# Optimization experiments

Hardware: AMD Instinct MI355X
Metric: run time of the kernel (lower is better)

Reference implementation:

```python
import jax, jax.numpy as jnp
import numpy as np

B = 32768
T = 1024  # num_time_bins


def setup_inputs() -> dict:
    key = jax.random.key(0)
    k1, k2, k3, k4 = jax.random.split(key, 4)
    hazard_values = jax.random.uniform(k1, (B, T), dtype=jnp.float32)
    labels_Y = jax.random.uniform(k2, (B,), dtype=jnp.float32) * T
    # nn.Linear(T, T): weight [T, T] (out, in), bias [T]
    lim = 1.0 / np.sqrt(T)
    W = jax.random.uniform(k3, (T, T), minval=-lim, maxval=lim, dtype=jnp.float32)
    b = jax.random.uniform(k4, (T,), minval=-lim, maxval=lim, dtype=jnp.float32)
    return {"hazard_values": hazard_values, "labels_Y": labels_Y, "W": W, "b": b}


def reference(hazard_values, labels_Y, W, b):
    # linear + sigmoid + argmax -> per-row truncation position
    logits = hazard_values @ W.T + b                       # [B, T]
    trunc_pos = jnp.argmax(jax.nn.sigmoid(logits), axis=1, keepdims=True)  # [B, 1] int
    # survival curve
    S = jnp.cumprod(1.0 - hazard_values, axis=1)           # [B, T]
    # vectorized truncation decay: for t >= p, multiply by exp(-(t - p))
    t = jnp.arange(T)[None, :]                             # [1, T]
    decay = jnp.where(t >= trunc_pos,
                      jnp.exp(-(t - trunc_pos).astype(S.dtype)),
                      jnp.ones((), S.dtype))
    S = S * decay
    # MSE between argmax position and labels (original prints; we skip prints)
    p = trunc_pos[:, 0].astype(jnp.float32)
    truncation_loss = jnp.mean((p - labels_Y) ** 2)
    return trunc_pos, S, truncation_loss
```

## Files before the change

### kernel.cpp

```cpp
#include <hip/hip_runtime.h>

#define B_ROWS 32768
#define T_BINS 1024

typedef __attribute__((ext_vector_type(8))) _Float16 half8;
typedef __attribute__((ext_vector_type(4))) float floatx4;

__device__ __forceinline__ unsigned long long pack_max(float v, int col) {
    unsigned x = __float_as_uint(v);
    x = (x & 0x80000000u) ? ~x : (x | 0x80000000u);
    return ((unsigned long long)x << 32) | (unsigned)(~col);
}

__device__ __forceinline__ void async16h(const _Float16* g, _Float16* l) {
    __builtin_amdgcn_global_load_lds(
        (const __attribute__((address_space(1))) unsigned int*)g,
        (__attribute__((address_space(3))) unsigned int*)l,
        16, 0, 0);
}

__global__ __launch_bounds__(256) void tof16_kernel(
    const float* __restrict__ src, _Float16* __restrict__ dst, int n4)
{
    int idx = blockIdx.x * 256 + threadIdx.x;
    if (idx >= n4) return;
    float4 x = ((const float4*)src)[idx];
    union { _Float16 h[4]; ushort4 u; } cv;
    cv.h[0] = (_Float16)x.x;
    cv.h[1] = (_Float16)x.y;
    cv.h[2] = (_Float16)x.z;
    cv.h[3] = (_Float16)x.w;
    ((ushort4*)dst)[idx] = cv.u;
}

__global__ __launch_bounds__(256, 2) void mega_kernel(
    const float* __restrict__ A, const _Float16* __restrict__ Wh,
    const float* __restrict__ bias, const float* __restrict__ labels,
    float* __restrict__ out_trunc, float* __restrict__ out_S,
    float* __restrict__ loss_acc)
{
    __shared__ _Float16 sA[2][64 * 64];
    __shared__ _Float16 sW[2][256 * 64];

    const int tid  = threadIdx.x;
    const int lane = tid & 63;
    const int wc   = tid >> 6;
    const int by   = blockIdx.x;

    const int arow = tid >> 2;
    const int ac   = tid & 3;
    const int x8a  = (arow ^ (arow >> 3)) & 7;
    const int sAw0 = arow * 64 + (((ac * 2) ^ x8a) * 8);
    const int sAw1 = arow * 64 + (((ac * 2 + 1) ^ x8a) * 8);
    const float* Abase = A + (size_t)(by * 64 + arow) * T_BINS + ac * 16;

    const int l3   = lane >> 3;
    const int wsl  = lane & 7;

    const int l15  = lane & 15;
    const int hi   = lane >> 4;
    const int xc   = (l15 & 7) ^ (l15 >> 3);

    float run_best[4][4];
    int   run_col[4][4];
#pragma unroll
    for (int i = 0; i < 4; ++i)
#pragma unroll
        for (int r = 0; r < 4; ++r) { run_best[i][r] = -3.4e38f; run_col[i][r] = 0; }

    {
        float4 f0 = *(const float4*)(Abase + 0);
        float4 f1 = *(const float4*)(Abase + 4);
        float4 f2 = *(const float4*)(Abase + 8);
        float4 f3 = *(const float4*)(Abase + 12);
        half8 h0, h1;
        h0[0] = (_Float16)f0.x; h0[1] = (_Float16)f0.y; h0[2] = (_Float16)f0.z; h0[3] = (_Float16)f0.w;
        h0[4] = (_Float16)f1.x; h0[5] = (_Float16)f1.y; h0[6] = (_Float16)f1.z; h0[7] = (_Float16)f1.w;
        h1[0] = (_Float16)f2.x; h1[1] = (_Float16)f2.y; h1[2] = (_Float16)f2.z; h1[3] = (_Float16)f2.w;
        h1[4] = (_Float16)f3.x; h1[5] = (_Float16)f3.y; h1[6] = (_Float16)f3.z; h1[7] = (_Float16)f3.w;
        *(half8*)&sA[0][sAw0] = h0;
        *(half8*)&sA[0][sAw1] = h1;
    }
#pragma unroll
    for (int r = 0; r < 8; ++r)
        async16h(Wh + (size_t)(wc * 64 + r * 8 + l3) * T_BINS + ((wsl ^ l3 ^ r) * 8),
                 &sW[0][(wc * 64 + r * 8) * 64]);
    float4 pa0 = *(const float4*)(Abase + 64);
    float4 pa1 = *(const float4*)(Abase + 68);
    float4 pa2 = *(const float4*)(Abase + 72);
    float4 pa3 = *(const float4*)(Abase + 76);
    __syncthreads();

    int n = 0;
    for (int bx = 0; bx < 4; ++bx) {
        const int colbase = bx * 256 + wc * 64 + l15;
        float bj[4];
#pragma unroll
        for (int j = 0; j < 4; ++j) bj[j] = bias[colbase + j * 16];

        floatx4 acc[4][4];
#pragma unroll
        for (int i = 0; i < 4; ++i)
#pragma unroll
            for (int j = 0; j < 4; ++j) acc[i][j] = (floatx4){0.f, 0.f, 0.f, 0.f};

        for (int t = 0; t < 16; ++t, ++n) {
            const int cur = n & 1;
            const int nxt = cur ^ 1;
            const int m   = (n + 1) & 63;
            const int bxn = m >> 4;
            const int k0n = (m & 15) * 64;

            const int kq = ((n + 2) & 15) * 64;
            float4 qa0 = *(const float4*)(Abase + kq + 0);
            float4 qa1 = *(const float4*)(Abase + kq + 4);
            float4 qa2 = *(const float4*)(Abase + kq + 8);
            float4 qa3 = *(const float4*)(Abase + kq + 12);

#pragma unroll
            for (int r = 0; r < 8; ++r)
                async16h(Wh + (size_t)(bxn * 256 + wc * 64 + r * 8 + l3) * T_BINS
                            + k0n + ((wsl ^ l3 ^ r) * 8),
                         &sW[nxt][(wc * 64 + r * 8) * 64]);

            {
                half8 h0, h1;
                h0[0] = (_Float16)pa0.x; h0[1] = (_Float16)pa0.y; h0[2] = (_Float16)pa0.z; h0[3] = (_Float16)pa0.w;
                h0[4] = (_Float16)pa1.x; h0[5] = (_Float16)pa1.y; h0[6] = (_Float16)pa1.z; h0[7] = (_Float16)pa1.w;
                h1[0] = (_Float16)pa2.x; h1[1] = (_Float16)pa2.y; h1[2] = (_Float16)pa2.z; h1[3] = (_Float16)pa2.w;
                h1[4] = (_Float16)pa3.x; h1[5] = (_Float16)pa3.y; h1[6] = (_Float16)pa3.z; h1[7] = (_Float16)pa3.w;
                *(half8*)&sA[nxt][sAw0] = h0;
                *(half8*)&sA[nxt][sAw1] = h1;
            }
            pa0 = qa0; pa1 = qa1; pa2 = qa2; pa3 = qa3;

#pragma unroll
            for (int g = 0; g < 2; ++g) {
                half8 ah[4], whf[4];
#pragma unroll
                for (int i = 0; i < 4; ++i)
                    ah[i] = *(const half8*)&sA[cur][(i * 16 + l15) * 64
                                                    + (((g * 4 + hi) ^ xc ^ (i * 2)) * 8)];
#pragma unroll
                for (int j = 0; j < 4; ++j)
                    whf[j] = *(const half8*)&sW[cur][(wc * 64 + j * 16 + l15) * 64
                                                     + (((g * 4 + hi) ^ xc ^ (j * 2)) * 8)];
#pragma unroll
                for (int i = 0; i < 4; ++i)
#pragma unroll
                    for (int j = 0; j < 4; ++j)
                        acc[i][j] = __builtin_amdgcn_mfma_f32_16x16x32_f16(ah[i], whf[j], acc[i][j], 0, 0, 0);
            }

            __syncthreads();
        }

#pragma unroll
        for (int i = 0; i < 4; ++i)
#pragma unroll
            for (int r = 0; r < 4; ++r)
#pragma unroll
                for (int j = 0; j < 4; ++j) {
                    float v = acc[i][j][r] + bj[j];
                    if (v > run_best[i][r]) { run_best[i][r] = v; run_col[i][r] = colbase + j * 16; }
                }
    }

    unsigned long long (*cand)[64] = reinterpret_cast<unsigned long long (*)[64]>(&sA[0][0]);
    float* trunc_s = reinterpret_cast<float*>(&sA[0][0]) + 512;

#pragma unroll
    for (int i = 0; i < 4; ++i)
#pragma unroll
        for (int r = 0; r < 4; ++r) {
            float best = run_best[i][r];
            int   bc   = run_col[i][r];
#pragma unroll
            for (int off = 8; off >= 1; off >>= 1) {
                float ov = __shfl_xor(best, off, 64);
                int   oc = __shfl_xor(bc, off, 64);
                if (ov > best || (ov == best && oc < bc)) { best = ov; bc = oc; }
            }
            if ((lane & 15) == 0)
                cand[wc][i * 16 + (lane >> 4) * 4 + r] = pack_max(best, bc);
        }
    __syncthreads();

    if (tid < 64) {
        unsigned long long m01 = cand[0][tid] > cand[1][tid] ? cand[0][tid] : cand[1][tid];
        unsigned long long m23 = cand[2][tid] > cand[3][tid] ? cand[2][tid] : cand[3][tid];
        unsigned long long mm = m01 > m23 ? m01 : m23;
        unsigned col = ~(unsigned)mm;
        float p = (float)col;
        int rowG = by * 64 + tid;
        out_trunc[rowG] = p;
        trunc_s[tid] = p;
        float d = p - labels[rowG];
        float term = d * d * (1.0f / (float)B_ROWS);
#pragma unroll
        for (int off = 32; off >= 1; off >>= 1)
            term += __shfl_down(term, off, 64);
        if (tid == 0) atomicAdd(loss_acc, term);
    }
    __syncthreads();

    for (int rr = 0; rr < 16; ++rr) {
        int row  = wc * 16 + rr;
        int rowG = by * 64 + row;
        const float* Hrow = A + (size_t)rowG * T_BINS + lane * 16;
        float4 h0 = *(const float4*)(Hrow + 0);
        float4 h1 = *(const float4*)(Hrow + 4);
        float4 h2 = *(const float4*)(Hrow + 8);
        float4 h3 = *(const float4*)(Hrow + 12);
        float hv[16] = {h0.x, h0.y, h0.z, h0.w, h1.x, h1.y, h1.z, h1.w,
                        h2.x, h2.y, h2.z, h2.w, h3.x, h3.y, h3.z, h3.w};
        float vprod[16];
        float run = 1.f;
#pragma unroll
        for (int j = 0; j < 16; ++j) { run *= (1.f - hv[j]); vprod[j] = run; }
        float x = run;
#pragma unroll
        for (int off = 1; off < 64; off <<= 1) {
            float o = __shfl_up(x, off, 64);
            if (lane >= off) x *= o;
        }
        float pre = __shfl_up(x, 1, 64);
        if (lane == 0) pre = 1.f;

        int p  = (int)trunc_s[row];
        int t0 = lane * 16;
        float sv[16];
#pragma unroll
        for (int j = 0; j < 16; ++j) {
            float s = pre * vprod[j];
            int t = t0 + j;
            if (t >= p) s *= __expf((float)(p - t));
            sv[j] = s;
        }
        float* Srow = out_S + (size_t)rowG * T_BINS + lane * 16;
        *(float4*)(Srow + 0)  = (float4){sv[0],  sv[1],  sv[2],  sv[3]};
        *(float4*)(Srow + 4)  = (float4){sv[4],  sv[5],  sv[6],  sv[7]};
        *(float4*)(Srow + 8)  = (float4){sv[8],  sv[9],  sv[10], sv[11]};
        *(float4*)(Srow + 12) = (float4){sv[12], sv[13], sv[14], sv[15]};
    }
}

#define BMf 64
#define BKf 16
#define LDSS (BMf + 4)
__global__ __launch_bounds__(256) void gemm_argmax_fp32(
    const float* __restrict__ A, const float* __restrict__ W,
    const float* __restrict__ bias, unsigned long long* __restrict__ rec)
{
    __shared__ float As[BKf][LDSS];
    __shared__ float Ws[BKf][LDSS];
    const int tid = threadIdx.x;
    const int tx = tid & 15, ty = tid >> 4;
    const int bx = blockIdx.x, by = blockIdx.y;
    const int ar = tid >> 2, ak = (tid & 3) << 2;
    const float* Arow = A + (size_t)(by * BMf + ar) * T_BINS + ak;
    const float* Wrow = W + (size_t)(bx * BMf + ar) * T_BINS + ak;
    float acc[4][4];
#pragma unroll
    for (int i = 0; i < 4; ++i)
#pragma unroll
        for (int j = 0; j < 4; ++j) acc[i][j] = 0.f;
    for (int k0 = 0; k0 < T_BINS; k0 += BKf) {
        float4 av = *(const float4*)(Arow + k0);
        float4 wvv = *(const float4*)(Wrow + k0);
        As[ak + 0][ar] = av.x; As[ak + 1][ar] = av.y; As[ak + 2][ar] = av.z; As[ak + 3][ar] = av.w;
        Ws[ak + 0][ar] = wvv.x; Ws[ak + 1][ar] = wvv.y; Ws[ak + 2][ar] = wvv.z; Ws[ak + 3][ar] = wvv.w;
        __syncthreads();
#pragma unroll
        for (int k = 0; k < BKf; ++k) {
            float4 a4 = *(const float4*)&As[k][ty * 4];
            float4 w4 = *(const float4*)&Ws[k][tx * 4];
            float aa[4] = {a4.x, a4.y, a4.z, a4.w};
            float ww[4] = {w4.x, w4.y, w4.z, w4.w};
#pragma unroll
            for (int i = 0; i < 4; ++i)
#pragma unroll
                for (int j = 0; j < 4; ++j) acc[i][j] = fmaf(aa[i], ww[j], acc[i][j]);
        }
        __syncthreads();
    }
    const int colBase = bx * BMf + tx * 4;
    float bv[4];
#pragma unroll
    for (int j = 0; j < 4; ++j) bv[j] = bias[colBase + j];
#pragma unroll
    for (int i = 0; i < 4; ++i) {
        float best = acc[i][0] + bv[0];
        int bc = colBase;
#pragma unroll
        for (int j = 1; j < 4; ++j) {
            float v = acc[i][j] + bv[j];
            if (v > best) { best = v; bc = colBase + j; }
        }
#pragma unroll
        for (int off = 8; off >= 1; off >>= 1) {
            float ov = __shfl_xor(best, off, 64);
            int oc = __shfl_xor(bc, off, 64);
            if (ov > best || (ov == best && oc < bc)) { best = ov; bc = oc; }
        }
        if (tx == 0) atomicMax(&rec[by * BMf + ty * 4 + i], pack_max(best, bc));
    }
}

__global__ __launch_bounds__(256) void finalize_kernel(
    const unsigned long long* __restrict__ rec, const float* __restrict__ labels,
    float* __restrict__ out_trunc, float* __restrict__ loss_acc)
{
    int i = blockIdx.x * 256 + threadIdx.x;
    unsigned col = ~(unsigned)(rec[i] & 0xFFFFFFFFull);
    float p = (float)col;
    out_trunc[i] = p;
    float d = p - labels[i];
    float term = d * d * (1.0f / (float)B_ROWS);
#pragma unroll
    for (int off = 32; off >= 1; off >>= 1)
        term += __shfl_down(term, off, 64);
    __shared__ float partials[4];
    int lane = threadIdx.x & 63, wv = threadIdx.x >> 6;
    if (lane == 0) partials[wv] = term;
    __syncthreads();
    if (threadIdx.x == 0)
        atomicAdd(loss_acc, partials[0] + partials[1] + partials[2] + partials[3]);
}

__global__ __launch_bounds__(256) void scan_kernel_f32(
    const float* __restrict__ H, const float* __restrict__ trunc_f,
    float* __restrict__ Sout)
{
    const int row = blockIdx.x;
    const int tid = threadIdx.x;
    const int lane = tid & 63;
    const int wv = tid >> 6;
    const float4 h = *(const float4*)(H + (size_t)row * T_BINS + tid * 4);
    float l0 = 1.f - h.x;
    float l1 = l0 * (1.f - h.y);
    float l2 = l1 * (1.f - h.z);
    float l3 = l2 * (1.f - h.w);
    float x = l3;
#pragma unroll
    for (int off = 1; off < 64; off <<= 1) {
        float o = __shfl_up(x, off, 64);
        if (lane >= off) x *= o;
    }
    float ex = __shfl_up(x, 1, 64);
    if (lane == 0) ex = 1.f;
    __shared__ float wtot[4];
    if (lane == 63) wtot[wv] = x;
    __syncthreads();
    float wpre = 1.f;
#pragma unroll
    for (int w = 0; w < 3; ++w)
        if (w < wv) wpre *= wtot[w];
    float pre = wpre * ex;
    int p = (int)trunc_f[row];
    int t0 = tid * 4;
    float sv[4] = {pre * l0, pre * l1, pre * l2, pre * l3};
#pragma unroll
    for (int j = 0; j < 4; ++j) {
        int t = t0 + j;
        if (t >= p) sv[j] *= __expf((float)(p - t));
    }
    float4 s4 = {sv[0], sv[1], sv[2], sv[3]};
    *(float4*)(Sout + (size_t)row * T_BINS + tid * 4) = s4;
}

extern "C" void kernel_launch(void* const* d_in, const int* in_sizes, int n_in,
                              void* d_out, int out_size, void* d_ws, size_t ws_size,
                              hipStream_t stream)
{
    const float* hazard = (const float*)d_in[0];
    const float* labels = (const float*)d_in[1];
    const float* W      = (const float*)d_in[2];
    const float* bias   = (const float*)d_in[3];

    float* out       = (float*)d_out;
    float* out_trunc = out;
    float* out_S     = out + B_ROWS;
    float* out_loss  = out + B_ROWS + (size_t)B_ROWS * T_BINS;

    hipMemsetAsync(out_loss, 0, sizeof(float), stream);

    const size_t NW = (size_t)T_BINS * T_BINS;
    if (ws_size >= NW * sizeof(_Float16)) {
        _Float16* Wh = (_Float16*)d_ws;
        tof16_kernel<<<(int)(NW / 4 / 256), 256, 0, stream>>>(W, Wh, (int)(NW / 4));
        mega_kernel<<<B_ROWS / 64, 256, 0, stream>>>(
            hazard, Wh, bias, labels, out_trunc, out_S, out_loss);
    } else {
        unsigned long long* rec = (unsigned long long*)out_S;
        hipMemsetAsync(rec, 0, (size_t)B_ROWS * sizeof(unsigned long long), stream);
        dim3 ggrid(T_BINS / BMf, B_ROWS / BMf);
        gemm_argmax_fp32<<<ggrid, 256, 0, stream>>>(hazard, W, bias, rec);
        finalize_kernel<<<B_ROWS / 256, 256, 0, stream>>>(rec, labels, out_trunc, out_loss);
        scan_kernel_f32<<<B_ROWS, 256, 0, stream>>>(hazard, out_trunc, out_S);
    }
}
```

Before: 352.8 us.

## Split fused kernel into large-tile fp16 GEMM-argmax and separate scan kernel

Replaces the single mega kernel with a 256x256-tile fp16 MFMA GEMM that reduces the per-row argmax across column quarters through 64-bit atomicMax records in workspace. A second kernel decodes the records, computes the loss and writes the truncated survival curves. The larger tiles raise operand reuse in the GEMM, and 512 blocks of 512 threads give better CU occupancy. In exchange, hazard is read twice from HBM and the mega kernel's overlap of the scan with the GEMM is lost.

```diff
diff --git a/kernel.cpp b/kernel.cpp
--- a/kernel.cpp
+++ b/kernel.cpp
@@ -31,6 +31,221 @@
     cv.h[2] = (_Float16)x.z;
     cv.h[3] = (_Float16)x.w;
     ((ushort4*)dst)[idx] = cv.u;
+}
+
+__global__ __launch_bounds__(512, 2) void gemm_argmax_f16(
+    const float* __restrict__ A, const _Float16* __restrict__ Wh,
+    const float* __restrict__ bias, unsigned long long* __restrict__ rec)
+{
+    __shared__ _Float16 sA[2][256 * 64];
+    __shared__ _Float16 sW[2][256 * 64];
+
+    const int tid  = threadIdx.x;
+    const int lane = tid & 63;
+    const int w    = tid >> 6;
+    const int wr   = w >> 1;
+    const int wcl  = w & 1;
+    const int slab = blockIdx.x >> 2;
+    const int cq   = blockIdx.x & 3;
+
+    const int arow = tid >> 1;
+    const int part = tid & 1;
+    const int x8a  = (arow ^ (arow >> 3)) & 7;
+    const float* Abase = A + (size_t)(slab * 256 + arow) * T_BINS;
+
+    const int l3  = lane >> 3;
+    const int wsl = lane & 7;
+
+    const int l15 = lane & 15;
+    const int hi  = lane >> 4;
+
+    floatx4 acc[4][8];
+#pragma unroll
+    for (int i = 0; i < 4; ++i)
+#pragma unroll
+        for (int j = 0; j < 8; ++j) acc[i][j] = (floatx4){0.f, 0.f, 0.f, 0.f};
+
+#pragma unroll
+    for (int s = 0; s < 4; ++s) {
+        int ps = part * 4 + s;
+        int sc = ps ^ x8a;
+        float4 f0 = *(const float4*)(Abase + sc * 8);
+        float4 f1 = *(const float4*)(Abase + sc * 8 + 4);
+        half8 hv;
+        hv[0] = (_Float16)f0.x; hv[1] = (_Float16)f0.y; hv[2] = (_Float16)f0.z; hv[3] = (_Float16)f0.w;
+        hv[4] = (_Float16)f1.x; hv[5] = (_Float16)f1.y; hv[6] = (_Float16)f1.z; hv[7] = (_Float16)f1.w;
+        *(half8*)&sA[0][arow * 64 + ps * 8] = hv;
+    }
+#pragma unroll
+    for (int r = 0; r < 4; ++r) {
+        int cl = w * 32 + r * 8 + l3;
+        int sk = wsl ^ ((cl ^ (cl >> 3)) & 7);
+        async16h(Wh + (size_t)(cq * 256 + cl) * T_BINS + sk * 8,
+                 &sW[0][(w * 32 + r * 8) * 64]);
+    }
+    __syncthreads();
+
+    for (int t = 0; t < 16; ++t) {
+        const int cur = t & 1;
+        const int nxt = cur ^ 1;
+        const int kn  = ((t + 1) & 15) * 64;
+
+        float4 qa0[4], qa1[4];
+#pragma unroll
+        for (int s = 0; s < 4; ++s) {
+            int sc = (part * 4 + s) ^ x8a;
+            qa0[s] = *(const float4*)(Abase + kn + sc * 8);
+            qa1[s] = *(const float4*)(Abase + kn + sc * 8 + 4);
+        }
+
+#pragma unroll
+        for (int r = 0; r < 4; ++r) {
+            int cl = w * 32 + r * 8 + l3;
+            int sk = wsl ^ ((cl ^ (cl >> 3)) & 7);
+            async16h(Wh + (size_t)(cq * 256 + cl) * T_BINS + kn + sk * 8,
+                     &sW[nxt][(w * 32 + r * 8) * 64]);
+        }
+
+#pragma unroll
+        for (int g = 0; g < 2; ++g) {
+            half8 ah[4];
+#pragma unroll
+            for (int i = 0; i < 4; ++i) {
+                int rl = wr * 64 + i * 16 + l15;
+                int xa = (rl ^ (rl >> 3)) & 7;
+                ah[i] = *(const half8*)&sA[cur][rl * 64 + (((g * 4 + hi) ^ xa) * 8)];
+            }
+#pragma unroll
+            for (int jb = 0; jb < 2; ++jb) {
+                half8 whf[4];
+#pragma unroll
+                for (int jj = 0; jj < 4; ++jj) {
+                    int cl = wcl * 128 + (jb * 4 + jj) * 16 + l15;
+                    int xw = (cl ^ (cl >> 3)) & 7;
+                    whf[jj] = *(const half8*)&sW[cur][cl * 64 + (((g * 4 + hi) ^ xw) * 8)];
+                }
+#pragma unroll
+                for (int i = 0; i < 4; ++i)
+#pragma unroll
+                    for (int jj = 0; jj < 4; ++jj)
+                        acc[i][jb * 4 + jj] = __builtin_amdgcn_mfma_f32_16x16x32_f16(
+                            ah[i], whf[jj], acc[i][jb * 4 + jj], 0, 0, 0);
+            }
+        }
+
+#pragma unroll
+        for (int s = 0; s < 4; ++s) {
+            half8 hv;
+            hv[0] = (_Float16)qa0[s].x; hv[1] = (_Float16)qa0[s].y;
+            hv[2] = (_Float16)qa0[s].z; hv[3] = (_Float16)qa0[s].w;
+            hv[4] = (_Float16)qa1[s].x; hv[5] = (_Float16)qa1[s].y;
+            hv[6] = (_Float16)qa1[s].z; hv[7] = (_Float16)qa1[s].w;
+            *(half8*)&sA[nxt][arow * 64 + (part * 4 + s) * 8] = hv;
+        }
+
+        __syncthreads();
+    }
+
+    const int colbase = cq * 256 + wcl * 128 + l15;
+    float bj[8];
+#pragma unroll
+    for (int j = 0; j < 8; ++j) bj[j] = bias[colbase + j * 16];
+
+    unsigned long long (*cand)[256] = reinterpret_cast<unsigned long long (*)[256]>(&sA[0][0]);
+
+#pragma unroll
+    for (int i = 0; i < 4; ++i)
+#pragma unroll
+        for (int r = 0; r < 4; ++r) {
+            float best = -3.4e38f;
+            int   bc   = 0;
+#pragma unroll
+            for (int j = 0; j < 8; ++j) {
+                float v = acc[i][j][r] + bj[j];
+                if (v > best) { best = v; bc = colbase + j * 16; }
+            }
+#pragma unroll
+            for (int off = 8; off >= 1; off >>= 1) {
+                float ov = __shfl_xor(best, off, 64);
+                int   oc = __shfl_xor(bc, off, 64);
+                if (ov > best || (ov == best && oc < bc)) { best = ov; bc = oc; }
+            }
+            if (l15 == 0)
+                cand[wcl][wr * 64 + i * 16 + hi * 4 + r] = pack_max(best, bc);
+        }
+    __syncthreads();
+
+    if (tid < 256) {
+        unsigned long long m0 = cand[0][tid], m1 = cand[1][tid];
+        atomicMax(&rec[slab * 256 + tid], m0 > m1 ? m0 : m1);
+    }
+}
+
+__global__ __launch_bounds__(256) void finscan_kernel(
+    const float* __restrict__ A, const unsigned long long* __restrict__ rec,
+    const float* __restrict__ labels, float* __restrict__ out_trunc,
+    float* __restrict__ out_S, float* __restrict__ loss_acc)
+{
+    __shared__ float trunc_s[64];
+    const int tid  = threadIdx.x;
+    const int lane = tid & 63;
+    const int wc   = tid >> 6;
+    const int by   = blockIdx.x;
+
+    if (tid < 64) {
+        int rowG = by * 64 + tid;
+        unsigned col = ~(unsigned)(rec[rowG] & 0xFFFFFFFFull);
+        float p = (float)col;
+        out_trunc[rowG] = p;
+        trunc_s[tid] = p;
+        float d = p - labels[rowG];
+        float term = d * d * (1.0f / (float)B_ROWS);
+#pragma unroll
+        for (int off = 32; off >= 1; off >>= 1)
+            term += __shfl_down(term, off, 64);
+        if (tid == 0) atomicAdd(loss_acc, term);
+    }
+    __syncthreads();
+
+    for (int rr = 0; rr < 16; ++rr) {
+        int row  = wc * 16 + rr;
+        int rowG = by * 64 + row;
+        const float* Hrow = A + (size_t)rowG * T_BINS + lane * 16;
+        float4 h0 = *(const float4*)(Hrow + 0);
+        float4 h1 = *(const float4*)(Hrow + 4);
+        float4 h2 = *(const float4*)(Hrow + 8);
+        float4 h3 = *(const float4*)(Hrow + 12);
+        float hv[16] = {h0.x, h0.y, h0.z, h0.w, h1.x, h1.y, h1.z, h1.w,
+                        h2.x, h2.y, h2.z, h2.w, h3.x, h3.y, h3.z, h3.w};
+        float vprod[16];
+        float run = 1.f;
+#pragma unroll
+        for (int j = 0; j < 16; ++j) { run *= (1.f - hv[j]); vprod[j] = run; }
+        float x = run;
+#pragma unroll
+        for (int off = 1; off < 64; off <<= 1) {
+            float o = __shfl_up(x, off, 64);
+            if (lane >= off) x *= o;
+        }
+        float pre = __shfl_up(x, 1, 64);
+        if (lane == 0) pre = 1.f;
+
+        int p  = (int)trunc_s[row];
+        int t0 = lane * 16;
+        float sv[16];
+#pragma unroll
+        for (int j = 0; j < 16; ++j) {
+            float s = pre * vprod[j];
+            int t = t0 + j;
+            if (t >= p) s *= __expf((float)(p - t));
+            sv[j] = s;
+        }
+        float* Srow = out_S + (size_t)rowG * T_BINS + lane * 16;
+        *(float4*)(Srow + 0)  = (float4){sv[0],  sv[1],  sv[2],  sv[3]};
+        *(float4*)(Srow + 4)  = (float4){sv[4],  sv[5],  sv[6],  sv[7]};
+        *(float4*)(Srow + 8)  = (float4){sv[8],  sv[9],  sv[10], sv[11]};
+        *(float4*)(Srow + 12) = (float4){sv[12], sv[13], sv[14], sv[15]};
+    }
 }
 
 __global__ __launch_bounds__(256, 2) void mega_kernel(
@@ -386,7 +601,17 @@
     hipMemsetAsync(out_loss, 0, sizeof(float), stream);
 
     const size_t NW = (size_t)T_BINS * T_BINS;
-    if (ws_size >= NW * sizeof(_Float16)) {
+    const size_t wh_bytes  = NW * sizeof(_Float16);
+    const size_t rec_bytes = (size_t)B_ROWS * sizeof(unsigned long long);
+
+    if (ws_size >= wh_bytes + rec_bytes) {
+        _Float16* Wh = (_Float16*)d_ws;
+        unsigned long long* rec = (unsigned long long*)((char*)d_ws + wh_bytes);
+        hipMemsetAsync(rec, 0, rec_bytes, stream);
+        tof16_kernel<<<(int)(NW / 4 / 256), 256, 0, stream>>>(W, Wh, (int)(NW / 4));
+        gemm_argmax_f16<<<512, 512, 0, stream>>>(hazard, Wh, bias, rec);
+        finscan_kernel<<<512, 256, 0, stream>>>(hazard, rec, labels, out_trunc, out_S, out_loss);
+    } else if (ws_size >= wh_bytes) {
         _Float16* Wh = (_Float16*)d_ws;
         tof16_kernel<<<(int)(NW / 4 / 256), 256, 0, stream>>>(W, Wh, (int)(NW / 4));
         mega_kernel<<<B_ROWS / 64, 256, 0, stream>>>(
```

After: 387.5 us. +9.8%, slower.
